# Kernel tuning notes

Measured on AMD Instinct MI355X. Metric: run time of the kernel, lower is better.

## Reference

```python
import jax, jax.numpy as jnp
import numpy as np

N_NODES = 50000
N_EDGES = 500000
N_REL = 50


def _linear(x, w, b):
    return x @ w.T + b


def _sage(x, src, dst, w_l, b_l, w_r, n_nodes):
    # PyG SAGEConv (mean aggr): out = lin_l(mean_{j in N(i)} x_j) + lin_r(x_i)
    msg = x[src]                                            # [E, F]
    s = jax.ops.segment_sum(msg, dst, num_segments=n_nodes)  # [N, F]
    cnt = jax.ops.segment_sum(jnp.ones((src.shape[0],), x.dtype), dst, num_segments=n_nodes)
    mean = s / jnp.clip(cnt, 1.0)[:, None]
    return mean @ w_l.T + b_l + x @ w_r.T


def setup_inputs() -> dict:
    key = jax.random.key(0)
    ks = jax.random.split(key, 24)

    def g(k, shape, fan_in):
        return jax.random.normal(k, shape, dtype=jnp.float32) * (1.0 / np.sqrt(fan_in))

    x = jax.random.normal(ks[0], (N_NODES, 16), dtype=jnp.float32)
    edge_index = jax.random.randint(ks[1], (2, N_EDGES), 0, N_NODES, dtype=jnp.int32)
    y = jax.random.randint(ks[2], (N_EDGES,), 0, N_REL, dtype=jnp.int32)

    return {
        "x": x, "edge_index": edge_index, "y": y,
        # SAGEConv 1: 16 -> 64
        "w1_l": g(ks[3], (64, 16), 16), "b1": jnp.zeros((64,), jnp.float32), "w1_r": g(ks[4], (64, 16), 16),
        # SAGEConv 2: 64 -> 128
        "w2_l": g(ks[5], (128, 64), 64), "b2": jnp.zeros((128,), jnp.float32), "w2_r": g(ks[6], (128, 64), 64),
        # object_fc: 256->128->64->32->16
        "of_w1": g(ks[7], (128, 256), 256), "of_b1": jnp.zeros((128,), jnp.float32),
        "of_w2": g(ks[8], (64, 128), 128), "of_b2": jnp.zeros((64,), jnp.float32),
        "of_w3": g(ks[9], (32, 64), 64), "of_b3": jnp.zeros((32,), jnp.float32),
        "of_w4": g(ks[10], (16, 32), 32), "of_b4": jnp.zeros((16,), jnp.float32),
        # relation_fc: 16->8->4->N_REL
        "rf_w1": g(ks[11], (8, 16), 16), "rf_b1": jnp.zeros((8,), jnp.float32),
        "rf_w2": g(ks[12], (4, 8), 8), "rf_b2": jnp.zeros((4,), jnp.float32),
        "rf_w3": g(ks[13], (N_REL, 4), 4), "rf_b3": jnp.zeros((N_REL,), jnp.float32),
    }


def reference(x, edge_index, y,
              w1_l, b1, w1_r, w2_l, b2, w2_r,
              of_w1, of_b1, of_w2, of_b2, of_w3, of_b3, of_w4, of_b4,
              rf_w1, rf_b1, rf_w2, rf_b2, rf_w3, rf_b3):
    src, dst = edge_index[0], edge_index[1]
    n = x.shape[0]

    h = jax.nn.relu(_sage(x, src, dst, w1_l, b1, w1_r, n))      # [N, 64]
    h = jax.nn.relu(_sage(h, src, dst, w2_l, b2, w2_r, n))      # [N, 128]

    # Batched version of the per-edge loop: gather endpoints, concat, MLP.
    feat = jnp.concatenate([h[src], h[dst]], axis=-1)           # [E, 256]
    o = jax.nn.relu(_linear(feat, of_w1, of_b1))   # dropout = identity (eval)
    o = jax.nn.relu(_linear(o, of_w2, of_b2))
    o = jax.nn.relu(_linear(o, of_w3, of_b3))
    o = _linear(o, of_w4, of_b4)                                # [E, 16]

    r = jax.nn.relu(_linear(o, rf_w1, rf_b1))
    r = jax.nn.relu(_linear(r, rf_w2, rf_b2))
    r = _linear(r, rf_w3, rf_b3)                                # [E, N_REL]
    return r, y
```

## Files before the change

### kernel.cpp

```cpp
#include <hip/hip_runtime.h>
#include <hip/hip_bf16.h>

#define N_NODES 50000
#define N_EDGES 500000
#define N_REL   50
#define NTILES  ((N_EDGES + 63) / 64)
#define EBLOCKS 1024
#define NODE_TILES ((N_NODES + 63) / 64)

#define CNTI_OFF   0
#define STARTS_OFF (CNTI_OFF + N_NODES)
#define CURSOR_OFF (STARTS_OFF + N_NODES)
#define SRCB_OFF   (CURSOR_OFF + N_NODES)
#define S1_OFF     (SRCB_OFF + N_EDGES)
#define S2_OFF     (S1_OFF + N_NODES*16)
#define H1_OFF     (S2_OFF + N_NODES*64)
#define H2_OFF     (H1_OFF + N_NODES*32)

typedef short short8  __attribute__((ext_vector_type(8)));
typedef short short4v __attribute__((ext_vector_type(4)));
typedef float f32x4   __attribute__((ext_vector_type(4)));
typedef float f4      __attribute__((ext_vector_type(4)));

#define MFMA16(a,b,c) __builtin_amdgcn_mfma_f32_16x16x32_bf16((a),(b),(c),0,0,0)

__device__ __forceinline__ short f2bf(float x) {
    unsigned u = __float_as_uint(x);
    unsigned r = (u + 0x7fffu + ((u >> 16) & 1u)) >> 16;
    return (short)r;
}
__device__ __forceinline__ float bf2f(short s) {
    return __uint_as_float(((unsigned)(unsigned short)s) << 16);
}

__device__ __forceinline__ short8 load_wfrag(const float* __restrict__ W, int row, int K, int k) {
    const f4* p = (const f4*)(W + (size_t)row * K + k);
    f4 a = p[0], b = p[1];
    short8 r;
    r[0] = f2bf(a[0]); r[1] = f2bf(a[1]); r[2] = f2bf(a[2]); r[3] = f2bf(a[3]);
    r[4] = f2bf(b[0]); r[5] = f2bf(b[1]); r[6] = f2bf(b[2]); r[7] = f2bf(b[3]);
    return r;
}


__global__ __launch_bounds__(256) void k_hist(
    const int* __restrict__ dst, int* __restrict__ cnt_i)
{
    int e = blockIdx.x * blockDim.x + threadIdx.x;
    if (e < N_EDGES) atomicAdd(&cnt_i[dst[e]], 1);
}

__global__ __launch_bounds__(1024) void k_scan(
    const int* __restrict__ cnt_i, int* __restrict__ starts, int* __restrict__ cursor)
{
    __shared__ int part[1024];
    const int i  = threadIdx.x;
    const int lo = i * 49;
    const int hi = min(N_NODES, lo + 49);
    int s = 0;
    for (int j = lo; j < hi; ++j) s += cnt_i[j];
    part[i] = s;
    __syncthreads();
    for (int d = 1; d < 1024; d <<= 1) {
        int v = (i >= d) ? part[i - d] : 0;
        __syncthreads();
        part[i] += v;
        __syncthreads();
    }
    int off = (i == 0) ? 0 : part[i - 1];
    for (int j = lo; j < hi; ++j) {
        starts[j] = off;
        cursor[j] = off;
        off += cnt_i[j];
    }
}

__global__ __launch_bounds__(256) void k_bucket(
    const int* __restrict__ src, const int* __restrict__ dst,
    int* __restrict__ cursor, int* __restrict__ srcb)
{
    int e = blockIdx.x * blockDim.x + threadIdx.x;
    if (e < N_EDGES) {
        int pos = atomicAdd(&cursor[dst[e]], 1);
        srcb[pos] = src[e];
    }
}


__global__ __launch_bounds__(256) void k_agg1(
    const float* __restrict__ x, const int* __restrict__ ebuf,
    const int* __restrict__ starts, const int* __restrict__ cnt_i,
    float* __restrict__ s1)
{
    int t = blockIdx.x * blockDim.x + threadIdx.x;
    if (t >= N_NODES * 16) return;
    int n = t >> 4, f = t & 15;
    int st = starts[n], c = cnt_i[n];
    float s = 0.0f;
    for (int i = 0; i < c; ++i) s += x[(size_t)ebuf[st + i] * 16 + f];
    s1[t] = s;
}

__global__ __launch_bounds__(256) void k_agg2(
    const short* __restrict__ h1b, const int* __restrict__ ebuf,
    const int* __restrict__ starts, const int* __restrict__ cnt_i,
    float* __restrict__ s2)
{
    int t = blockIdx.x * blockDim.x + threadIdx.x;
    if (t >= N_NODES * 64) return;
    int n = t >> 6, f = t & 63;
    int st = starts[n], c = cnt_i[n];
    float s = 0.0f;
    for (int i = 0; i < c; ++i) s += bf2f(h1b[(size_t)ebuf[st + i] * 64 + f]);
    s2[t] = s;
}

__global__ __launch_bounds__(256) void k_sage1_mfma(
    const float* __restrict__ x, const float* __restrict__ s1,
    const int* __restrict__ cnt_i,
    const float* __restrict__ w1_l, const float* __restrict__ b1,
    const float* __restrict__ w1_r, short* __restrict__ h1b)
{
    __shared__ short feat[64 * 40];

    const int t    = threadIdx.x;
    const int w    = t >> 6;
    const int lane = t & 63;
    const int lr   = lane & 15;
    const int lg   = lane >> 4;
    const int base = blockIdx.x * 64;

    short8 w1f;
    if (lg < 2) w1f = load_wfrag(w1_l, w * 16 + lr, 16, lg * 8);
    else        w1f = load_wfrag(w1_r, w * 16 + lr, 16, (lg - 2) * 8);

    {
        int e  = t >> 2, q = t & 3;
        int ng = base + e;
        short8 v = (short8)0;
        if (ng < N_NODES) {
            if (q < 2) {
                int ci = cnt_i[ng];
                float inv = 1.0f / (float)(ci > 0 ? ci : 1);
                f4 a = *(const f4*)(s1 + (size_t)ng * 16 + q * 8);
                f4 b = *(const f4*)(s1 + (size_t)ng * 16 + q * 8 + 4);
#pragma unroll
                for (int j = 0; j < 4; ++j) { v[j] = f2bf(a[j] * inv); v[4 + j] = f2bf(b[j] * inv); }
            } else {
                f4 a = *(const f4*)(x + (size_t)ng * 16 + (q - 2) * 8);
                f4 b = *(const f4*)(x + (size_t)ng * 16 + (q - 2) * 8 + 4);
#pragma unroll
                for (int j = 0; j < 4; ++j) { v[j] = f2bf(a[j]); v[4 + j] = f2bf(b[j]); }
            }
        }
        *(short8*)&feat[e * 40 + q * 8] = v;
    }
    __syncthreads();

    f32x4 acc[4];
    f4 bia = *(const f4*)&b1[w * 16 + lg * 4];
#pragma unroll
    for (int nt = 0; nt < 4; ++nt) {
        acc[nt][0] = bia[0]; acc[nt][1] = bia[1]; acc[nt][2] = bia[2]; acc[nt][3] = bia[3];
    }
#pragma unroll
    for (int nt = 0; nt < 4; ++nt) {
        int e = nt * 16 + lr;
        short8 bf = *(const short8*)&feat[e * 40 + lg * 8];
        acc[nt] = MFMA16(w1f, bf, acc[nt]);
    }
#pragma unroll
    for (int nt = 0; nt < 4; ++nt) {
        int ng = base + nt * 16 + lr;
        if (ng < N_NODES) {
            short4v o;
#pragma unroll
            for (int r = 0; r < 4; ++r) { float v = acc[nt][r]; o[r] = f2bf(v > 0.0f ? v : 0.0f); }
            *(short4v*)&h1b[(size_t)ng * 64 + w * 16 + lg * 4] = o;
        }
    }
}

__global__ __launch_bounds__(256) void k_sage2p(
    const short* __restrict__ h1b, const float* __restrict__ s2,
    const int* __restrict__ cnt_i,
    const float* __restrict__ w2_l, const float* __restrict__ b2,
    const float* __restrict__ w2_r, const float* __restrict__ ow1,
    short* __restrict__ plb, short* __restrict__ prb)
{
    __shared__ short feat[64 * 128];
    __shared__ short feat2[64 * 128];

    const int t    = threadIdx.x;
    const int w    = t >> 6;
    const int lane = t & 63;
    const int lr   = lane & 15;
    const int lg   = lane >> 4;
    const int base = blockIdx.x * 64;

    short8 wf[2][4];
#pragma unroll
    for (int mt = 0; mt < 2; ++mt)
#pragma unroll
        for (int kt = 0; kt < 4; ++kt) {
            int row = w * 32 + mt * 16 + lr;
            int k   = kt * 32 + lg * 8;
            wf[mt][kt] = (k < 64) ? load_wfrag(w2_r, row, 64, k)
                                  : load_wfrag(w2_l, row, 64, k - 64);
        }

    {
        int e  = t >> 2, q = t & 3;
        int ng = base + e;
        if (q < 2) {
            const short* hp = (ng < N_NODES) ? (h1b + (size_t)ng * 64 + q * 32) : nullptr;
#pragma unroll
            for (int j = 0; j < 4; ++j) {
                short8 v = hp ? *(const short8*)(hp + j * 8) : (short8)0;
                int scol = (q * 32 + j * 8) ^ ((e & 7) << 3);
                *(short8*)&feat[e * 128 + scol] = v;
            }
        } else {
            float inv = 1.0f;
            const float* srcp = nullptr;
            if (ng < N_NODES) {
                int ci = cnt_i[ng];
                inv = 1.0f / (float)(ci > 0 ? ci : 1);
                srcp = s2 + (size_t)ng * 64 + (q - 2) * 32;
            }
#pragma unroll
            for (int j = 0; j < 4; ++j) {
                short8 v = (short8)0;
                if (srcp) {
                    f4 a = *(const f4*)(srcp + j * 8);
                    f4 b = *(const f4*)(srcp + j * 8 + 4);
#pragma unroll
                    for (int q2 = 0; q2 < 4; ++q2) { v[q2] = f2bf(a[q2] * inv); v[4 + q2] = f2bf(b[q2] * inv); }
                }
                int scol = ((q - 2) * 32 + 64 + j * 8) ^ ((e & 7) << 3);
                *(short8*)&feat[e * 128 + scol] = v;
            }
        }
    }
    __syncthreads();

    {
        f32x4 acc[2][4];
#pragma unroll
        for (int mt = 0; mt < 2; ++mt) {
            f4 bia = *(const f4*)&b2[w * 32 + mt * 16 + lg * 4];
#pragma unroll
            for (int nt = 0; nt < 4; ++nt) {
                acc[mt][nt][0] = bia[0]; acc[mt][nt][1] = bia[1];
                acc[mt][nt][2] = bia[2]; acc[mt][nt][3] = bia[3];
            }
        }
#pragma unroll
        for (int kt = 0; kt < 4; ++kt) {
            short8 bf[4];
#pragma unroll
            for (int nt = 0; nt < 4; ++nt) {
                int e = nt * 16 + lr;
                int scol = (kt * 32 + lg * 8) ^ ((e & 7) << 3);
                bf[nt] = *(const short8*)&feat[e * 128 + scol];
            }
#pragma unroll
            for (int mt = 0; mt < 2; ++mt)
#pragma unroll
                for (int nt = 0; nt < 4; ++nt)
                    acc[mt][nt] = MFMA16(wf[mt][kt], bf[nt], acc[mt][nt]);
        }
#pragma unroll
        for (int mt = 0; mt < 2; ++mt)
#pragma unroll
            for (int nt = 0; nt < 4; ++nt) {
                int e  = nt * 16 + lr;
                int n0 = w * 32 + mt * 16 + lg * 4;
                short4v s;
#pragma unroll
                for (int r = 0; r < 4; ++r) {
                    float v = acc[mt][nt][r];
                    s[r] = f2bf(v > 0.0f ? v : 0.0f);
                }
                *(short4v*)&feat2[e * 128 + (n0 ^ ((e & 7) << 3))] = s;
            }
    }
    __syncthreads();

    short8 wfL[2][4], wfR[2][4];
#pragma unroll
    for (int mt = 0; mt < 2; ++mt)
#pragma unroll
        for (int kt = 0; kt < 4; ++kt) {
            int row = w * 32 + mt * 16 + lr;
            int k   = kt * 32 + lg * 8;
            wfL[mt][kt] = load_wfrag(ow1, row, 256, k);
            wfR[mt][kt] = load_wfrag(ow1, row, 256, 128 + k);
        }
    f32x4 aL[2][4], aR[2][4];
#pragma unroll
    for (int mt = 0; mt < 2; ++mt)
#pragma unroll
        for (int nt = 0; nt < 4; ++nt) { aL[mt][nt] = (f32x4)0.0f; aR[mt][nt] = (f32x4)0.0f; }
#pragma unroll
    for (int kt = 0; kt < 4; ++kt) {
        short8 bf[4];
#pragma unroll
        for (int nt = 0; nt < 4; ++nt) {
            int e = nt * 16 + lr;
            int scol = (kt * 32 + lg * 8) ^ ((e & 7) << 3);
            bf[nt] = *(const short8*)&feat2[e * 128 + scol];
        }
#pragma unroll
        for (int mt = 0; mt < 2; ++mt)
#pragma unroll
            for (int nt = 0; nt < 4; ++nt) {
                aL[mt][nt] = MFMA16(wfL[mt][kt], bf[nt], aL[mt][nt]);
                aR[mt][nt] = MFMA16(wfR[mt][kt], bf[nt], aR[mt][nt]);
            }
    }
#pragma unroll
    for (int mt = 0; mt < 2; ++mt)
#pragma unroll
        for (int nt = 0; nt < 4; ++nt) {
            int ng = base + nt * 16 + lr;
            if (ng < N_NODES) {
                int n0 = w * 32 + mt * 16 + lg * 4;
                short4v oL, oR;
#pragma unroll
                for (int r = 0; r < 4; ++r) { oL[r] = f2bf(aL[mt][nt][r]); oR[r] = f2bf(aR[mt][nt][r]); }
                *(short4v*)&plb[(size_t)ng * 128 + n0] = oL;
                *(short4v*)&prb[(size_t)ng * 128 + n0] = oR;
            }
        }
}

__global__ __launch_bounds__(256) void k_ycopy(
    const int* __restrict__ y, float* __restrict__ out)
{
    int e = blockIdx.x * blockDim.x + threadIdx.x;
    if (e < N_EDGES) out[(size_t)N_EDGES * N_REL + e] = (float)y[e];
}

__global__ __launch_bounds__(256, 4) void k_edge3(
    const short* __restrict__ plb, const short* __restrict__ prb,
    const int* __restrict__ src, const int* __restrict__ dst,
    const float* __restrict__ ob1,
    const float* __restrict__ ow2, const float* __restrict__ ob2,
    const float* __restrict__ ow3, const float* __restrict__ ob3,
    const float* __restrict__ ow4, const float* __restrict__ ob4,
    const float* __restrict__ rw1, const float* __restrict__ rb1,
    const float* __restrict__ rw2, const float* __restrict__ rb2,
    const float* __restrict__ rw3, const float* __restrict__ rb3,
    float* __restrict__ out)
{
    __shared__ short a1s[64 * 128];
    __shared__ short actB[64 * 96];
    __shared__ float sw[662];

    short* act2  = actB;
    short* act3  = actB + 64 * 64;
    float* tailf = (float*)a1s;

    const int t    = threadIdx.x;
    const int w    = t >> 6;
    const int lane = t & 63;
    const int lr   = lane & 15;
    const int lg   = lane >> 4;

    if (t < 128) sw[t]       = ob1[t];
    if (t < 64)  sw[128 + t] = ob2[t];
    if (t < 32)  sw[192 + t] = ob3[t];
    if (t < 16)  sw[224 + t] = ob4[t];
    if (t < 8)   sw[240 + t] = rb1[t];
    if (t < 4)   sw[248 + t] = rb2[t];
    if (t < 50)  sw[252 + t] = rb3[t];
    if (t < 128) sw[302 + t] = rw1[t];
    if (t < 32)  sw[430 + t] = rw2[t];
    if (t < 200) sw[462 + t] = rw3[t];

    short8 w2f[4];
#pragma unroll
    for (int kt = 0; kt < 4; ++kt)
        w2f[kt] = load_wfrag(ow2, w * 16 + lr, 128, kt * 32 + lg * 8);

    short8 w3f[2][2];
#pragma unroll
    for (int mt = 0; mt < 2; ++mt)
#pragma unroll
        for (int kt = 0; kt < 2; ++kt)
            w3f[mt][kt] = load_wfrag(ow3, mt * 16 + lr, 64, kt * 32 + lg * 8);

    short8 w4f = load_wfrag(ow4, lr, 32, lg * 8);

    __syncthreads();

    const int e = t >> 2, p = t & 3;
    short8 vl0, vl1, vl2, vl3, vr0, vr1, vr2, vr3;

#define LOADTILE(TI)                                                        \
    {                                                                       \
        int eg  = (TI) * 64 + e;                                            \
        int egc = eg < N_EDGES ? eg : N_EDGES - 1;                          \
        int sn = src[egc], dn = dst[egc];                                   \
        const short8* plp = (const short8*)(plb + (size_t)sn * 128 + p * 32); \
        const short8* prp = (const short8*)(prb + (size_t)dn * 128 + p * 32); \
        vl0 = plp[0]; vl1 = plp[1]; vl2 = plp[2]; vl3 = plp[3];             \
        vr0 = prp[0]; vr1 = prp[1]; vr2 = prp[2]; vr3 = prp[3];             \
    }

    LOADTILE(blockIdx.x)

    for (int tile = blockIdx.x; tile < NTILES; tile += EBLOCKS) {
        const int base = tile * 64;

        {
            short8 VL[4] = {vl0, vl1, vl2, vl3};
            short8 VR[4] = {vr0, vr1, vr2, vr3};
#pragma unroll
            for (int j = 0; j < 4; ++j) {
                short8 s;
#pragma unroll
                for (int i = 0; i < 8; ++i) {
                    float v = bf2f(VL[j][i]) + bf2f(VR[j][i]) + sw[p * 32 + j * 8 + i];
                    s[i] = f2bf(v > 0.0f ? v : 0.0f);
                }
                int scol = (p * 32 + j * 8) ^ ((e & 7) << 3);
                *(short8*)&a1s[e * 128 + scol] = s;
            }
        }
        __syncthreads();

        if (tile + EBLOCKS < NTILES) LOADTILE(tile + EBLOCKS)

        {
            f32x4 acc[4];
            f32x4 bia;
#pragma unroll
            for (int r = 0; r < 4; ++r) bia[r] = sw[128 + w * 16 + lg * 4 + r];
#pragma unroll
            for (int nt = 0; nt < 4; ++nt) acc[nt] = bia;
#pragma unroll
            for (int kt = 0; kt < 4; ++kt) {
#pragma unroll
                for (int nt = 0; nt < 4; ++nt) {
                    int en = nt * 16 + lr;
                    int scol = (kt * 32 + lg * 8) ^ ((en & 7) << 3);
                    short8 bf = *(const short8*)&a1s[en * 128 + scol];
                    acc[nt] = MFMA16(w2f[kt], bf, acc[nt]);
                }
            }
#pragma unroll
            for (int nt = 0; nt < 4; ++nt) {
                int en = nt * 16 + lr;
                int n0 = w * 16 + lg * 4;
                short4v s;
#pragma unroll
                for (int r = 0; r < 4; ++r) {
                    float v = acc[nt][r];
                    s[r] = f2bf(v > 0.0f ? v : 0.0f);
                }
                *(short4v*)&act2[en * 64 + (n0 ^ ((en & 7) << 3))] = s;
            }
        }
        __syncthreads();

        {
            const int e3 = w * 16 + lr;
            float* T = tailf + w * 512;

            f32x4 acc[2];
#pragma unroll
            for (int mt = 0; mt < 2; ++mt)
#pragma unroll
                for (int r = 0; r < 4; ++r) acc[mt][r] = sw[192 + mt * 16 + lg * 4 + r];
#pragma unroll
            for (int kt = 0; kt < 2; ++kt) {
                int scol = (kt * 32 + lg * 8) ^ ((e3 & 7) << 3);
                short8 bf = *(const short8*)&act2[e3 * 64 + scol];
#pragma unroll
                for (int mt = 0; mt < 2; ++mt)
                    acc[mt] = MFMA16(w3f[mt][kt], bf, acc[mt]);
            }
#pragma unroll
            for (int mt = 0; mt < 2; ++mt) {
                short4v s;
#pragma unroll
                for (int r = 0; r < 4; ++r) {
                    float v = acc[mt][r];
                    s[r] = f2bf(v > 0.0f ? v : 0.0f);
                }
                *(short4v*)&act3[e3 * 32 + mt * 16 + lg * 4] = s;
            }
            __builtin_amdgcn_wave_barrier();

            {
                short8 bf = *(const short8*)&act3[e3 * 32 + lg * 8];
                f32x4 a4;
#pragma unroll
                for (int r = 0; r < 4; ++r) a4[r] = sw[224 + lg * 4 + r];
                a4 = MFMA16(w4f, bf, a4);
#pragma unroll
                for (int r = 0; r < 4; ++r) T[lr * 17 + lg * 4 + r] = a4[r];
            }
            __builtin_amdgcn_wave_barrier();

            {
                float af[16];
#pragma unroll
                for (int f = 0; f < 16; ++f) af[f] = T[lr * 17 + f];
#pragma unroll
                for (int oo = 0; oo < 2; ++oo) {
                    int o = lg * 2 + oo;
                    float v = sw[240 + o];
#pragma unroll
                    for (int f = 0; f < 16; ++f) v += af[f] * sw[302 + o * 16 + f];
                    T[272 + lr * 9 + o] = v > 0.0f ? v : 0.0f;
                }
            }
            __builtin_amdgcn_wave_barrier();

            {
                float v = sw[248 + lg];
#pragma unroll
                for (int f = 0; f < 8; ++f) v += T[272 + lr * 9 + f] * sw[430 + lg * 8 + f];
                T[416 + lr * 5 + lg] = v > 0.0f ? v : 0.0f;
            }
            __builtin_amdgcn_wave_barrier();

            size_t obase = (size_t)(base + w * 16) * N_REL;
#pragma unroll
            for (int k2 = 0; k2 < 13; ++k2) {
                int idx = k2 * 64 + lane;
                if (idx < 16 * N_REL) {
                    int el = idx / N_REL;
                    int o  = idx - el * N_REL;
                    if (base + w * 16 + el < N_EDGES) {
                        float v = sw[252 + o];
#pragma unroll
                        for (int f = 0; f < 4; ++f) v += T[416 + el * 5 + f] * sw[462 + o * 4 + f];
                        out[obase + idx] = v;
                    }
                }
            }
        }
        __syncthreads();
    }
#undef LOADTILE
}

extern "C" void kernel_launch(void* const* d_in, const int* in_sizes, int n_in,
                              void* d_out, int out_size, void* d_ws, size_t ws_size,
                              hipStream_t stream) {
    const float* x    = (const float*)d_in[0];
    const int*   ei   = (const int*)d_in[1];
    const int*   src  = ei;
    const int*   dst  = ei + N_EDGES;
    const int*   y    = (const int*)d_in[2];
    const float* w1_l = (const float*)d_in[3];
    const float* b1   = (const float*)d_in[4];
    const float* w1_r = (const float*)d_in[5];
    const float* w2_l = (const float*)d_in[6];
    const float* b2   = (const float*)d_in[7];
    const float* w2_r = (const float*)d_in[8];
    const float* ow1  = (const float*)d_in[9];
    const float* ob1  = (const float*)d_in[10];
    const float* ow2  = (const float*)d_in[11];
    const float* ob2  = (const float*)d_in[12];
    const float* ow3  = (const float*)d_in[13];
    const float* ob3  = (const float*)d_in[14];
    const float* ow4  = (const float*)d_in[15];
    const float* ob4  = (const float*)d_in[16];
    const float* rw1  = (const float*)d_in[17];
    const float* rb1  = (const float*)d_in[18];
    const float* rw2  = (const float*)d_in[19];
    const float* rb2  = (const float*)d_in[20];
    const float* rw3  = (const float*)d_in[21];
    const float* rb3  = (const float*)d_in[22];

    float* ws     = (float*)d_ws;
    int*   cnt_i  = (int*)(ws + CNTI_OFF);
    int*   starts = (int*)(ws + STARTS_OFF);
    int*   cursor = (int*)(ws + CURSOR_OFF);
    int*   srcb   = (int*)(ws + SRCB_OFF);
    float* s1     = ws + S1_OFF;
    float* s2     = ws + S2_OFF;
    short* h1b    = (short*)(ws + H1_OFF);
    short* plb    = (short*)(ws + H2_OFF);
    short* prb    = (short*)(ws + S2_OFF);
    float* out    = (float*)d_out;

    hipMemsetAsync(cnt_i, 0, N_NODES * sizeof(int), stream);

    k_hist  <<<(N_EDGES + 255) / 256, 256, 0, stream>>>(dst, cnt_i);
    k_scan  <<<1, 1024, 0, stream>>>(cnt_i, starts, cursor);
    k_bucket<<<(N_EDGES + 255) / 256, 256, 0, stream>>>(src, dst, cursor, srcb);

    k_agg1<<<(N_NODES * 16 + 255) / 256, 256, 0, stream>>>(x, srcb, starts, cnt_i, s1);
    k_sage1_mfma<<<NODE_TILES, 256, 0, stream>>>(x, s1, cnt_i, w1_l, b1, w1_r, h1b);

    k_agg2<<<(N_NODES * 64 + 255) / 256, 256, 0, stream>>>(h1b, srcb, starts, cnt_i, s2);
    k_sage2p<<<NODE_TILES, 256, 0, stream>>>(h1b, s2, cnt_i, w2_l, b2, w2_r, ow1, plb, prb);

    k_ycopy<<<(N_EDGES + 255) / 256, 256, 0, stream>>>(y, out);

    k_edge3<<<EBLOCKS, 256, 0, stream>>>(
        plb, prb, src, dst,
        ob1, ow2, ob2, ow3, ob3, ow4, ob4,
        rw1, rb1, rw2, rb2, rw3, rb3, out);
}
```

Before: 446.5 us.

## Fuse neighbor aggregation into SAGE MFMA kernels and merge label copy into histogram

Removes the separate aggregation kernels (agg1, agg2) and instead gathers and sums neighbor features directly inside the SAGE MFMA kernels, so the fp32 s1/s2 intermediates are never written or re-read. It also folds the y-to-float copy into the histogram kernel, cutting two kernel launches plus the intermediate traffic. The cost is parallelism: each gathering thread now loops over a whole node's neighbor list with 8 or 32 accumulators instead of one feature per thread. That raises register pressure and per-thread serial latency on the gather.

```diff
diff --git a/kernel.cpp b/kernel.cpp
--- a/kernel.cpp
+++ b/kernel.cpp
@@ -12,10 +12,9 @@
 #define STARTS_OFF (CNTI_OFF + N_NODES)
 #define CURSOR_OFF (STARTS_OFF + N_NODES)
 #define SRCB_OFF   (CURSOR_OFF + N_NODES)
-#define S1_OFF     (SRCB_OFF + N_EDGES)
-#define S2_OFF     (S1_OFF + N_NODES*16)
-#define H1_OFF     (S2_OFF + N_NODES*64)
-#define H2_OFF     (H1_OFF + N_NODES*32)
+#define PRB_OFF    (SRCB_OFF + N_EDGES)
+#define H1_OFF     (PRB_OFF + N_NODES*32)
+#define PLB_OFF    (H1_OFF + N_NODES*32)
 
 typedef short short8  __attribute__((ext_vector_type(8)));
 typedef short short4v __attribute__((ext_vector_type(4)));
@@ -43,11 +42,15 @@
 }
 
 
-__global__ __launch_bounds__(256) void k_hist(
-    const int* __restrict__ dst, int* __restrict__ cnt_i)
+__global__ __launch_bounds__(256) void k_histy(
+    const int* __restrict__ dst, int* __restrict__ cnt_i,
+    const int* __restrict__ y, float* __restrict__ out)
 {
     int e = blockIdx.x * blockDim.x + threadIdx.x;
-    if (e < N_EDGES) atomicAdd(&cnt_i[dst[e]], 1);
+    if (e < N_EDGES) {
+        atomicAdd(&cnt_i[dst[e]], 1);
+        out[(size_t)N_EDGES * N_REL + e] = (float)y[e];
+    }
 }
 
 __global__ __launch_bounds__(1024) void k_scan(
@@ -86,38 +89,9 @@
     }
 }
 
-
-__global__ __launch_bounds__(256) void k_agg1(
-    const float* __restrict__ x, const int* __restrict__ ebuf,
+__global__ __launch_bounds__(256) void k_sage1g(
+    const float* __restrict__ x, const int* __restrict__ srcb,
     const int* __restrict__ starts, const int* __restrict__ cnt_i,
-    float* __restrict__ s1)
-{
-    int t = blockIdx.x * blockDim.x + threadIdx.x;
-    if (t >= N_NODES * 16) return;
-    int n = t >> 4, f = t & 15;
-    int st = starts[n], c = cnt_i[n];
-    float s = 0.0f;
-    for (int i = 0; i < c; ++i) s += x[(size_t)ebuf[st + i] * 16 + f];
-    s1[t] = s;
-}
-
-__global__ __launch_bounds__(256) void k_agg2(
-    const short* __restrict__ h1b, const int* __restrict__ ebuf,
-    const int* __restrict__ starts, const int* __restrict__ cnt_i,
-    float* __restrict__ s2)
-{
-    int t = blockIdx.x * blockDim.x + threadIdx.x;
-    if (t >= N_NODES * 64) return;
-    int n = t >> 6, f = t & 63;
-    int st = starts[n], c = cnt_i[n];
-    float s = 0.0f;
-    for (int i = 0; i < c; ++i) s += bf2f(h1b[(size_t)ebuf[st + i] * 64 + f]);
-    s2[t] = s;
-}
-
-__global__ __launch_bounds__(256) void k_sage1_mfma(
-    const float* __restrict__ x, const float* __restrict__ s1,
-    const int* __restrict__ cnt_i,
     const float* __restrict__ w1_l, const float* __restrict__ b1,
     const float* __restrict__ w1_r, short* __restrict__ h1b)
 {
@@ -140,12 +114,18 @@
         short8 v = (short8)0;
         if (ng < N_NODES) {
             if (q < 2) {
-                int ci = cnt_i[ng];
-                float inv = 1.0f / (float)(ci > 0 ? ci : 1);
-                f4 a = *(const f4*)(s1 + (size_t)ng * 16 + q * 8);
-                f4 b = *(const f4*)(s1 + (size_t)ng * 16 + q * 8 + 4);
-#pragma unroll
-                for (int j = 0; j < 4; ++j) { v[j] = f2bf(a[j] * inv); v[4 + j] = f2bf(b[j] * inv); }
+                int st = starts[ng], c = cnt_i[ng];
+                float acc[8] = {0, 0, 0, 0, 0, 0, 0, 0};
+                for (int i = 0; i < c; ++i) {
+                    const float* xp = x + (size_t)srcb[st + i] * 16 + q * 8;
+                    f4 a = *(const f4*)xp;
+                    f4 b = *(const f4*)(xp + 4);
+#pragma unroll
+                    for (int j = 0; j < 4; ++j) { acc[j] += a[j]; acc[4 + j] += b[j]; }
+                }
+                float inv = 1.0f / (float)(c > 0 ? c : 1);
+#pragma unroll
+                for (int j = 0; j < 8; ++j) v[j] = f2bf(acc[j] * inv);
             } else {
                 f4 a = *(const f4*)(x + (size_t)ng * 16 + (q - 2) * 8);
                 f4 b = *(const f4*)(x + (size_t)ng * 16 + (q - 2) * 8 + 4);
@@ -181,9 +161,9 @@
     }
 }
 
-__global__ __launch_bounds__(256) void k_sage2p(
-    const short* __restrict__ h1b, const float* __restrict__ s2,
-    const int* __restrict__ cnt_i,
+__global__ __launch_bounds__(256) void k_sage2g(
+    const short* __restrict__ h1b, const int* __restrict__ srcb,
+    const int* __restrict__ starts, const int* __restrict__ cnt_i,
     const float* __restrict__ w2_l, const float* __restrict__ b2,
     const float* __restrict__ w2_r, const float* __restrict__ ow1,
     short* __restrict__ plb, short* __restrict__ prb)
@@ -221,23 +201,32 @@
                 *(short8*)&feat[e * 128 + scol] = v;
             }
         } else {
-            float inv = 1.0f;
-            const float* srcp = nullptr;
+            float acc[32];
+#pragma unroll
+            for (int j = 0; j < 32; ++j) acc[j] = 0.0f;
+            int c = 0;
             if (ng < N_NODES) {
-                int ci = cnt_i[ng];
-                inv = 1.0f / (float)(ci > 0 ? ci : 1);
-                srcp = s2 + (size_t)ng * 64 + (q - 2) * 32;
-            }
-#pragma unroll
-            for (int j = 0; j < 4; ++j) {
-                short8 v = (short8)0;
-                if (srcp) {
-                    f4 a = *(const f4*)(srcp + j * 8);
-                    f4 b = *(const f4*)(srcp + j * 8 + 4);
-#pragma unroll
-                    for (int q2 = 0; q2 < 4; ++q2) { v[q2] = f2bf(a[q2] * inv); v[4 + q2] = f2bf(b[q2] * inv); }
-                }
-                int scol = ((q - 2) * 32 + 64 + j * 8) ^ ((e & 7) << 3);
+                int st = starts[ng];
+                c = cnt_i[ng];
+                for (int i = 0; i < c; ++i) {
+                    const short8* hp = (const short8*)(h1b + (size_t)srcb[st + i] * 64 + (q - 2) * 32);
+                    short8 a0 = hp[0], a1 = hp[1], a2 = hp[2], a3 = hp[3];
+#pragma unroll
+                    for (int j = 0; j < 8; ++j) {
+                        acc[j]      += bf2f(a0[j]);
+                        acc[8 + j]  += bf2f(a1[j]);
+                        acc[16 + j] += bf2f(a2[j]);
+                        acc[24 + j] += bf2f(a3[j]);
+                    }
+                }
+            }
+            float inv = 1.0f / (float)(c > 0 ? c : 1);
+#pragma unroll
+            for (int jj = 0; jj < 4; ++jj) {
+                short8 v;
+#pragma unroll
+                for (int j = 0; j < 8; ++j) v[j] = f2bf(acc[jj * 8 + j] * inv);
+                int scol = ((q - 2) * 32 + 64 + jj * 8) ^ ((e & 7) << 3);
                 *(short8*)&feat[e * 128 + scol] = v;
             }
         }
@@ -333,13 +322,6 @@
                 *(short4v*)&prb[(size_t)ng * 128 + n0] = oR;
             }
         }
-}
-
-__global__ __launch_bounds__(256) void k_ycopy(
-    const int* __restrict__ y, float* __restrict__ out)
-{
-    int e = blockIdx.x * blockDim.x + threadIdx.x;
-    if (e < N_EDGES) out[(size_t)N_EDGES * N_REL + e] = (float)y[e];
 }
 
 __global__ __launch_bounds__(256, 4) void k_edge3(
@@ -583,26 +565,20 @@
     int*   starts = (int*)(ws + STARTS_OFF);
     int*   cursor = (int*)(ws + CURSOR_OFF);
     int*   srcb   = (int*)(ws + SRCB_OFF);
-    float* s1     = ws + S1_OFF;
-    float* s2     = ws + S2_OFF;
+    short* prb    = (short*)(ws + PRB_OFF);
     short* h1b    = (short*)(ws + H1_OFF);
-    short* plb    = (short*)(ws + H2_OFF);
-    short* prb    = (short*)(ws + S2_OFF);
+    short* plb    = (short*)(ws + PLB_OFF);
     float* out    = (float*)d_out;
 
     hipMemsetAsync(cnt_i, 0, N_NODES * sizeof(int), stream);
 
-    k_hist  <<<(N_EDGES + 255) / 256, 256, 0, stream>>>(dst, cnt_i);
+    k_histy <<<(N_EDGES + 255) / 256, 256, 0, stream>>>(dst, cnt_i, y, out);
     k_scan  <<<1, 1024, 0, stream>>>(cnt_i, starts, cursor);
     k_bucket<<<(N_EDGES + 255) / 256, 256, 0, stream>>>(src, dst, cursor, srcb);
 
-    k_agg1<<<(N_NODES * 16 + 255) / 256, 256, 0, stream>>>(x, srcb, starts, cnt_i, s1);
-    k_sage1_mfma<<<NODE_TILES, 256, 0, stream>>>(x, s1, cnt_i, w1_l, b1, w1_r, h1b);
-
-    k_agg2<<<(N_NODES * 64 + 255) / 256, 256, 0, stream>>>(h1b, srcb, starts, cnt_i, s2);
-    k_sage2p<<<NODE_TILES, 256, 0, stream>>>(h1b, s2, cnt_i, w2_l, b2, w2_r, ow1, plb, prb);
-
-    k_ycopy<<<(N_EDGES + 255) / 256, 256, 0, stream>>>(y, out);
+    k_sage1g<<<NODE_TILES, 256, 0, stream>>>(x, srcb, starts, cnt_i, w1_l, b1, w1_r, h1b);
+    k_sage2g<<<NODE_TILES, 256, 0, stream>>>(h1b, srcb, starts, cnt_i,
+                                             w2_l, b2, w2_r, ow1, plb, prb);
 
     k_edge3<<<EBLOCKS, 256, 0, stream>>>(
         plb, prb, src, dst,
```

After: 411.0 us. 7.9% less time.
